# Kernel tuning notes

Measured on AMD Instinct MI355X. Metric: run time of the kernel, lower is better.

Reference implementation:

```python
import jax, jax.numpy as jnp
import numpy as np

N = 50000   # nodes
E = 800000  # edges
F_IN, F_HID, F_OUT = 128, 96, 40


def setup_inputs() -> dict:
    key = jax.random.key(0)
    ks = jax.random.split(key, 9)
    x = jax.random.normal(ks[0], (N, F_IN), dtype=jnp.float32)
    edge_index = jax.random.randint(ks[1], (2, E), 0, N, dtype=jnp.int32)
    def lin(k, fi, fo):
        s = 1.0 / np.sqrt(fi)
        return jax.random.uniform(k, (fi, fo), jnp.float32, -s, s)
    W1 = lin(ks[2], F_IN, F_HID)
    b1 = jnp.zeros((F_HID,), jnp.float32)
    W2 = lin(ks[3], F_HID, F_HID)
    b2 = jnp.zeros((F_HID,), jnp.float32)
    Wout = lin(ks[4], F_HID, F_OUT)
    bout = jnp.zeros((F_OUT,), jnp.float32)
    return {"x": x, "edge_index": edge_index, "W1": W1, "b1": b1,
            "W2": W2, "b2": b2, "Wout": Wout, "bout": bout}


def _gcn_norm(edge_index, n):
    # add self-loops, symmetric degree normalization (PyG GCNConv default)
    loops = jnp.arange(n, dtype=edge_index.dtype)
    src = jnp.concatenate([edge_index[0], loops])
    dst = jnp.concatenate([edge_index[1], loops])
    deg = jax.ops.segment_sum(jnp.ones_like(dst, dtype=jnp.float32), dst,
                              num_segments=n)
    dinv = jnp.where(deg > 0, jax.lax.rsqrt(deg), 0.0)
    norm = dinv[src] * dinv[dst]   # [E+N]
    return src, dst, norm


def _gcn_layer(h, src, dst, norm, W, b, n):
    # linear transform, then normalized scatter-add aggregation, then bias
    h = h @ W                                 # [N, Fout]
    msg = h[src] * norm[:, None]              # gather + scale
    agg = jax.ops.segment_sum(msg, dst, num_segments=n)
    return agg + b


def reference(x, edge_index, W1, b1, W2, b2, Wout, bout):
    n = x.shape[0]
    src, dst, norm = _gcn_norm(edge_index, n)
    h = jax.nn.relu(_gcn_layer(x, src, dst, norm, W1, b1, n))
    h = jax.nn.relu(_gcn_layer(h, src, dst, norm, W2, b2, n))
    return h @ Wout + bout
```

## Files before the change

kernel.cpp:

```cpp
#include <hip/hip_runtime.h>
#include <hip/hip_fp16.h>

#define N_NODES 50000
#define N_EDGES 800000
#define F_INN   128
#define F_HID   96
#define F_OUTT  40


__global__ void count_kernel(const int* __restrict__ dst, int* __restrict__ counts,
                             int* __restrict__ rank, int e) {
    int i = blockIdx.x * blockDim.x + threadIdx.x;
    if (i < e) rank[i] = atomicAdd(&counts[dst[i]], 1);
}

__global__ __launch_bounds__(1024) void scan_local_kernel(
        const int* __restrict__ counts, int* __restrict__ row_start,
        float* __restrict__ dinv, int* __restrict__ blk_sums, int n) {
    __shared__ int wave_sums[16];
    int tid = threadIdx.x, lane = tid & 63, wid = tid >> 6;
    int i = blockIdx.x * 1024 + tid;
    int v = (i < n) ? counts[i] : 0;
    int val = v;
    #pragma unroll
    for (int off = 1; off < 64; off <<= 1) {
        int u = __shfl_up(val, off, 64);
        if (lane >= off) val += u;
    }
    if (lane == 63) wave_sums[wid] = val;
    __syncthreads();
    if (wid == 0) {
        int w = (lane < 16) ? wave_sums[lane] : 0;
        #pragma unroll
        for (int off = 1; off < 16; off <<= 1) {
            int u = __shfl_up(w, off, 64);
            if (lane >= off) w += u;
        }
        if (lane < 16) wave_sums[lane] = w;
    }
    __syncthreads();
    int excl = ((wid == 0) ? 0 : wave_sums[wid - 1]) + (val - v);
    if (i < n) {
        row_start[i] = excl;
        dinv[i] = rsqrtf((float)(v + 1));
    }
    if (tid == 0) blk_sums[blockIdx.x] = wave_sums[15];
}

__global__ void scan_blk_kernel(const int* __restrict__ blk_sums, int* __restrict__ blk_off,
                                int* __restrict__ row_start, int n, int nblk) {
    int lane = threadIdx.x;
    int v = (lane < nblk) ? blk_sums[lane] : 0;
    int val = v;
    #pragma unroll
    for (int off = 1; off < 64; off <<= 1) {
        int u = __shfl_up(val, off, 64);
        if (lane >= off) val += u;
    }
    if (lane < nblk) blk_off[lane] = val - v;
    if (lane == 63) row_start[n] = val;
}

__global__ __launch_bounds__(1024) void scan_apply_kernel(
        int* __restrict__ row_start, const int* __restrict__ blk_off, int n) {
    int i = blockIdx.x * 1024 + threadIdx.x;
    if (i < n) row_start[i] += blk_off[blockIdx.x];
}

__global__ void fill_csr_kernel(const int* __restrict__ src, const int* __restrict__ dst,
                                const int* __restrict__ rank, const int* __restrict__ row_start,
                                int* __restrict__ csr_src, int e) {
    int i = blockIdx.x * blockDim.x + threadIdx.x;
    if (i >= e) return;
    csr_src[row_start[dst[i]] + rank[i]] = src[i];
}


template <int FI>
__global__ __launch_bounds__(384) void gemm96_kernel(
        const float* __restrict__ A, const float* __restrict__ W,
        const float* __restrict__ dinv, __half2* __restrict__ C, int n) {
    __shared__ float Wlds[FI * 96];
    int tid = threadIdx.y * 24 + threadIdx.x;
    for (int i = tid; i < FI * 24; i += 384)
        reinterpret_cast<float4*>(Wlds)[i] = reinterpret_cast<const float4*>(W)[i];
    __syncthreads();

    int j  = threadIdx.x * 4;
    int n0 = blockIdx.x * 64 + threadIdx.y;
    int nn[4];
    #pragma unroll
    for (int t = 0; t < 4; ++t) nn[t] = min(n0 + 16 * t, n - 1);

    float4 acc[4];
    #pragma unroll
    for (int t = 0; t < 4; ++t) acc[t] = make_float4(0.f, 0.f, 0.f, 0.f);

    for (int k = 0; k < FI; k += 4) {
        float4 a[4];
        #pragma unroll
        for (int t = 0; t < 4; ++t)
            a[t] = *reinterpret_cast<const float4*>(A + (size_t)nn[t] * FI + k);
        float4 w0 = *reinterpret_cast<const float4*>(Wlds + (k + 0) * 96 + j);
        float4 w1 = *reinterpret_cast<const float4*>(Wlds + (k + 1) * 96 + j);
        float4 w2 = *reinterpret_cast<const float4*>(Wlds + (k + 2) * 96 + j);
        float4 w3 = *reinterpret_cast<const float4*>(Wlds + (k + 3) * 96 + j);
        #pragma unroll
        for (int t = 0; t < 4; ++t) {
            acc[t].x += a[t].x * w0.x + a[t].y * w1.x + a[t].z * w2.x + a[t].w * w3.x;
            acc[t].y += a[t].x * w0.y + a[t].y * w1.y + a[t].z * w2.y + a[t].w * w3.y;
            acc[t].z += a[t].x * w0.z + a[t].y * w1.z + a[t].z * w2.z + a[t].w * w3.z;
            acc[t].w += a[t].x * w0.w + a[t].y * w1.w + a[t].z * w2.w + a[t].w * w3.w;
        }
    }
    #pragma unroll
    for (int t = 0; t < 4; ++t) {
        int node = n0 + 16 * t;
        if (node < n) {
            float dn = dinv[node];
            __half2 h01 = __floats2half2_rn(acc[t].x * dn, acc[t].y * dn);
            __half2 h23 = __floats2half2_rn(acc[t].z * dn, acc[t].w * dn);
            __half2* Cp = C + (size_t)node * 48 + (j >> 1);
            Cp[0] = h01;
            Cp[1] = h23;
        }
    }
}

__global__ __launch_bounds__(320) void gemm_out_kernel(
        const float* __restrict__ A, const float* __restrict__ W,
        const float* __restrict__ bias, float* __restrict__ C, int n) {
    __shared__ float Wlds[96 * 40];
    int tid = threadIdx.y * 10 + threadIdx.x;
    for (int i = tid; i < 96 * 10; i += 320)
        reinterpret_cast<float4*>(Wlds)[i] = reinterpret_cast<const float4*>(W)[i];
    __syncthreads();

    int j    = threadIdx.x * 4;
    int node = blockIdx.x * 32 + threadIdx.y;
    int nc   = min(node, n - 1);
    float4 acc = make_float4(0.f, 0.f, 0.f, 0.f);
    for (int k = 0; k < 96; k += 4) {
        float4 a = *reinterpret_cast<const float4*>(A + (size_t)nc * 96 + k);
        float4 w0 = *reinterpret_cast<const float4*>(Wlds + (k + 0) * 40 + j);
        float4 w1 = *reinterpret_cast<const float4*>(Wlds + (k + 1) * 40 + j);
        float4 w2 = *reinterpret_cast<const float4*>(Wlds + (k + 2) * 40 + j);
        float4 w3 = *reinterpret_cast<const float4*>(Wlds + (k + 3) * 40 + j);
        acc.x += a.x * w0.x + a.y * w1.x + a.z * w2.x + a.w * w3.x;
        acc.y += a.x * w0.y + a.y * w1.y + a.z * w2.y + a.w * w3.y;
        acc.z += a.x * w0.z + a.y * w1.z + a.z * w2.z + a.w * w3.z;
        acc.w += a.x * w0.w + a.y * w1.w + a.z * w2.w + a.w * w3.w;
    }
    if (node < n) {
        float4 b = *reinterpret_cast<const float4*>(bias + j);
        acc.x += b.x; acc.y += b.y; acc.z += b.z; acc.w += b.w;
        *reinterpret_cast<float4*>(C + (size_t)node * 40 + j) = acc;
    }
}


__global__ __launch_bounds__(256) void agg_kernel(
        const __half2* __restrict__ T, const int* __restrict__ row_start,
        const int* __restrict__ csr_src, const float* __restrict__ dinv,
        const float* __restrict__ bias, float* __restrict__ H, int n) {
    int lane = threadIdx.x & 63;
    int node = __builtin_amdgcn_readfirstlane(blockIdx.x * 4 + (threadIdx.x >> 6));
    if (node >= n) return;
    int fl = min(lane, 47);

    float2 self = __half22float2(T[(size_t)node * 48 + fl]);
    float accx = self.x, accy = self.y;

    int idx = row_start[node];
    int end = row_start[node + 1];
    for (; idx + 4 <= end; idx += 4) {
        int s0 = csr_src[idx + 0];
        int s1 = csr_src[idx + 1];
        int s2 = csr_src[idx + 2];
        int s3 = csr_src[idx + 3];
        __half2 a0 = T[(size_t)s0 * 48 + fl];
        __half2 a1 = T[(size_t)s1 * 48 + fl];
        __half2 a2 = T[(size_t)s2 * 48 + fl];
        __half2 a3 = T[(size_t)s3 * 48 + fl];
        float2 f0 = __half22float2(a0);
        float2 f1 = __half22float2(a1);
        float2 f2 = __half22float2(a2);
        float2 f3 = __half22float2(a3);
        accx += f0.x + f1.x + f2.x + f3.x;
        accy += f0.y + f1.y + f2.y + f3.y;
    }
    for (; idx < end; ++idx) {
        float2 f = __half22float2(T[(size_t)csr_src[idx] * 48 + fl]);
        accx += f.x; accy += f.y;
    }
    if (lane < 48) {
        float dn = dinv[node];
        float2 b = reinterpret_cast<const float2*>(bias)[lane];
        float2 o;
        o.x = fmaxf(dn * accx + b.x, 0.f);
        o.y = fmaxf(dn * accy + b.y, 0.f);
        reinterpret_cast<float2*>(H)[(size_t)node * 48 + lane] = o;
    }
}


extern "C" void kernel_launch(void* const* d_in, const int* in_sizes, int n_in,
                              void* d_out, int out_size, void* d_ws, size_t ws_size,
                              hipStream_t stream) {
    const float* x    = (const float*)d_in[0];
    const int*   ei   = (const int*)d_in[1];
    const float* W1   = (const float*)d_in[2];
    const float* b1   = (const float*)d_in[3];
    const float* W2   = (const float*)d_in[4];
    const float* b2   = (const float*)d_in[5];
    const float* Wout = (const float*)d_in[6];
    const float* bout = (const float*)d_in[7];
    float*       out  = (float*)d_out;

    const int* src = ei;
    const int* dst = ei + N_EDGES;

    char* ws = (char*)d_ws;
    size_t off = 0;
    auto alloc = [&](size_t bytes) {
        size_t o = off;
        off = (off + bytes + 511) & ~(size_t)511;
        return (void*)(ws + o);
    };
    int*     counts    = (int*)    alloc(N_NODES * sizeof(int));
    int*     row_start = (int*)    alloc((N_NODES + 1) * sizeof(int));
    float*   dinv      = (float*)  alloc(N_NODES * sizeof(float));
    int*     blk_sums  = (int*)    alloc(64 * sizeof(int));
    int*     blk_off   = (int*)    alloc(64 * sizeof(int));
    int*     rank      = (int*)    alloc((size_t)N_EDGES * sizeof(int));
    int*     csr_src   = (int*)    alloc((size_t)N_EDGES * sizeof(int));
    __half2* Th        = (__half2*)alloc((size_t)N_NODES * 48 * sizeof(__half2));
    float*   Hf        = (float*)  alloc((size_t)N_NODES * F_HID * sizeof(float));

    const int NSCAN = (N_NODES + 1023) / 1024;

    hipMemsetAsync(counts, 0, N_NODES * sizeof(int), stream);
    count_kernel<<<(N_EDGES + 255) / 256, 256, 0, stream>>>(dst, counts, rank, N_EDGES);
    scan_local_kernel<<<NSCAN, 1024, 0, stream>>>(counts, row_start, dinv, blk_sums, N_NODES);
    scan_blk_kernel<<<1, 64, 0, stream>>>(blk_sums, blk_off, row_start, N_NODES, NSCAN);
    scan_apply_kernel<<<NSCAN, 1024, 0, stream>>>(row_start, blk_off, N_NODES);
    fill_csr_kernel<<<(N_EDGES + 255) / 256, 256, 0, stream>>>(
        src, dst, rank, row_start, csr_src, N_EDGES);

    gemm96_kernel<F_INN><<<(N_NODES + 63) / 64, dim3(24, 16), 0, stream>>>(
        x, W1, dinv, Th, N_NODES);
    agg_kernel<<<(N_NODES + 3) / 4, 256, 0, stream>>>(
        Th, row_start, csr_src, dinv, b1, Hf, N_NODES);

    gemm96_kernel<F_HID><<<(N_NODES + 63) / 64, dim3(24, 16), 0, stream>>>(
        Hf, W2, dinv, Th, N_NODES);
    agg_kernel<<<(N_NODES + 3) / 4, 256, 0, stream>>>(
        Th, row_start, csr_src, dinv, b2, Hf, N_NODES);

    gemm_out_kernel<<<(N_NODES + 31) / 32, dim3(10, 32), 0, stream>>>(
        Hf, Wout, bout, out, N_NODES);
}
```

Baseline: 271.7 us.

## Use MFMA fp16 GEMMs, spread degree-count atomics, unroll aggregation gathers

Replaces the scalar FMA hidden-layer GEMMs with MFMA 16x16x32 fp16 kernels. The weights are pre-transposed to padded fp16 by a new small kernel, and outputs are staged through LDS so the global stores are coalesced. Degree counting now spreads atomics over four sub-counters per node to reduce contention, with per-sub-bucket bases computed in scan_apply. The aggregation inner loop is unrolled from 4 to 8 gathers for more memory-level parallelism. Rounding the GEMM inputs to fp16 adds precision risk.

```diff
diff --git a/kernel.cpp b/kernel.cpp
--- a/kernel.cpp
+++ b/kernel.cpp
@@ -7,20 +7,27 @@
 #define F_HID   96
 #define F_OUTT  40
 
-
-__global__ void count_kernel(const int* __restrict__ dst, int* __restrict__ counts,
+typedef _Float16 half8 __attribute__((ext_vector_type(8)));
+typedef float    floatx4 __attribute__((ext_vector_type(4)));
+
+
+__global__ void count_kernel(const int* __restrict__ dst, int* __restrict__ counts4,
                              int* __restrict__ rank, int e) {
     int i = blockIdx.x * blockDim.x + threadIdx.x;
-    if (i < e) rank[i] = atomicAdd(&counts[dst[i]], 1);
+    if (i < e) rank[i] = atomicAdd(&counts4[dst[i] * 4 + (i & 3)], 1);
 }
 
 __global__ __launch_bounds__(1024) void scan_local_kernel(
-        const int* __restrict__ counts, int* __restrict__ row_start,
+        const int4* __restrict__ counts4, int* __restrict__ row_start,
         float* __restrict__ dinv, int* __restrict__ blk_sums, int n) {
     __shared__ int wave_sums[16];
     int tid = threadIdx.x, lane = tid & 63, wid = tid >> 6;
     int i = blockIdx.x * 1024 + tid;
-    int v = (i < n) ? counts[i] : 0;
+    int v = 0;
+    if (i < n) {
+        int4 c = counts4[i];
+        v = c.x + c.y + c.z + c.w;
+    }
     int val = v;
     #pragma unroll
     for (int off = 1; off < 64; off <<= 1) {
@@ -62,68 +69,95 @@
 }
 
 __global__ __launch_bounds__(1024) void scan_apply_kernel(
-        int* __restrict__ row_start, const int* __restrict__ blk_off, int n) {
+        int* __restrict__ row_start, const int* __restrict__ blk_off,
+        const int4* __restrict__ counts4, int4* __restrict__ base4, int n) {
     int i = blockIdx.x * 1024 + threadIdx.x;
-    if (i < n) row_start[i] += blk_off[blockIdx.x];
+    if (i >= n) return;
+    int4 c = counts4[i];
+    int b = row_start[i] + blk_off[blockIdx.x];
+    row_start[i] = b;
+    base4[i] = make_int4(b, b + c.x, b + c.x + c.y, b + c.x + c.y + c.z);
 }
 
 __global__ void fill_csr_kernel(const int* __restrict__ src, const int* __restrict__ dst,
-                                const int* __restrict__ rank, const int* __restrict__ row_start,
+                                const int* __restrict__ rank, const int* __restrict__ base4,
                                 int* __restrict__ csr_src, int e) {
     int i = blockIdx.x * blockDim.x + threadIdx.x;
     if (i >= e) return;
-    csr_src[row_start[dst[i]] + rank[i]] = src[i];
-}
-
+    csr_src[base4[dst[i] * 4 + (i & 3)] + rank[i]] = src[i];
+}
+
+__global__ void wt_kernel(const float* __restrict__ W1, const float* __restrict__ W2,
+                          __half* __restrict__ BT1, __half* __restrict__ BT2) {
+    int i = blockIdx.x * 256 + threadIdx.x;
+    if (i < 96 * 128) {
+        int j = i / 128, k = i - j * 128;
+        BT1[j * 136 + k] = __float2half(W1[k * 96 + j]);
+    } else if (i < 96 * 128 + 96 * 96) {
+        int t = i - 96 * 128;
+        int j = t / 96, k = t - j * 96;
+        BT2[j * 136 + k] = __float2half(W2[k * 96 + j]);
+    }
+}
 
 template <int FI>
-__global__ __launch_bounds__(384) void gemm96_kernel(
-        const float* __restrict__ A, const float* __restrict__ W,
-        const float* __restrict__ dinv, __half2* __restrict__ C, int n) {
-    __shared__ float Wlds[FI * 96];
-    int tid = threadIdx.y * 24 + threadIdx.x;
-    for (int i = tid; i < FI * 24; i += 384)
-        reinterpret_cast<float4*>(Wlds)[i] = reinterpret_cast<const float4*>(W)[i];
-    __syncthreads();
-
-    int j  = threadIdx.x * 4;
-    int n0 = blockIdx.x * 64 + threadIdx.y;
-    int nn[4];
-    #pragma unroll
-    for (int t = 0; t < 4; ++t) nn[t] = min(n0 + 16 * t, n - 1);
-
-    float4 acc[4];
-    #pragma unroll
-    for (int t = 0; t < 4; ++t) acc[t] = make_float4(0.f, 0.f, 0.f, 0.f);
-
-    for (int k = 0; k < FI; k += 4) {
-        float4 a[4];
-        #pragma unroll
-        for (int t = 0; t < 4; ++t)
-            a[t] = *reinterpret_cast<const float4*>(A + (size_t)nn[t] * FI + k);
-        float4 w0 = *reinterpret_cast<const float4*>(Wlds + (k + 0) * 96 + j);
-        float4 w1 = *reinterpret_cast<const float4*>(Wlds + (k + 1) * 96 + j);
-        float4 w2 = *reinterpret_cast<const float4*>(Wlds + (k + 2) * 96 + j);
-        float4 w3 = *reinterpret_cast<const float4*>(Wlds + (k + 3) * 96 + j);
-        #pragma unroll
-        for (int t = 0; t < 4; ++t) {
-            acc[t].x += a[t].x * w0.x + a[t].y * w1.x + a[t].z * w2.x + a[t].w * w3.x;
-            acc[t].y += a[t].x * w0.y + a[t].y * w1.y + a[t].z * w2.y + a[t].w * w3.y;
-            acc[t].z += a[t].x * w0.z + a[t].y * w1.z + a[t].z * w2.z + a[t].w * w3.z;
-            acc[t].w += a[t].x * w0.w + a[t].y * w1.w + a[t].z * w2.w + a[t].w * w3.w;
+__global__ __launch_bounds__(256) void mfma_gemm_kernel(
+        const float* __restrict__ X, const __half* __restrict__ BTg,
+        const float* __restrict__ dinv, float4* __restrict__ Th4, int n) {
+    __shared__ __half BTl[96 * 136];
+    __shared__ __half OUTl[4 * 16 * 104];
+    int tid = threadIdx.x;
+    {
+        const int4* s = reinterpret_cast<const int4*>(BTg);
+        int4* d = reinterpret_cast<int4*>(BTl);
+        for (int i = tid; i < 96 * 136 / 8; i += 256) d[i] = s[i];
+    }
+    __syncthreads();
+
+    int lane = tid & 63, w = tid >> 6;
+    int lm = lane & 15, q = lane >> 4;
+    int base = blockIdx.x * 64 + w * 16;
+    int node = base + lm;
+    int nclamp = min(node, n - 1);
+    const float* Xrow = X + (size_t)nclamp * FI;
+
+    floatx4 cf[6];
+    #pragma unroll
+    for (int t = 0; t < 6; ++t) cf[t] = (floatx4){0.f, 0.f, 0.f, 0.f};
+
+    constexpr int KS = FI / 32;
+    #pragma unroll
+    for (int ks = 0; ks < KS; ++ks) {
+        const float4* xr = reinterpret_cast<const float4*>(Xrow + 32 * ks + q * 8);
+        float4 f0 = xr[0], f1 = xr[1];
+        union { half8 v; __half2 h[4]; } b;
+        b.h[0] = __floats2half2_rn(f0.x, f0.y);
+        b.h[1] = __floats2half2_rn(f0.z, f0.w);
+        b.h[2] = __floats2half2_rn(f1.x, f1.y);
+        b.h[3] = __floats2half2_rn(f1.z, f1.w);
+        #pragma unroll
+        for (int t = 0; t < 6; ++t) {
+            half8 a = *reinterpret_cast<const half8*>(
+                &BTl[(t * 16 + lm) * 136 + q * 8 + 32 * ks]);
+            cf[t] = __builtin_amdgcn_mfma_f32_16x16x32_f16(a, b.v, cf[t], 0, 0, 0);
         }
     }
-    #pragma unroll
-    for (int t = 0; t < 4; ++t) {
-        int node = n0 + 16 * t;
-        if (node < n) {
-            float dn = dinv[node];
-            __half2 h01 = __floats2half2_rn(acc[t].x * dn, acc[t].y * dn);
-            __half2 h23 = __floats2half2_rn(acc[t].z * dn, acc[t].w * dn);
-            __half2* Cp = C + (size_t)node * 48 + (j >> 1);
-            Cp[0] = h01;
-            Cp[1] = h23;
-        }
+
+    float dn = dinv[nclamp];
+    __half* orow = OUTl + (w * 16 + lm) * 104;
+    #pragma unroll
+    for (int t = 0; t < 6; ++t) {
+        union { int2 i2; __half2 h[2]; } u;
+        u.h[0] = __floats2half2_rn(cf[t][0] * dn, cf[t][1] * dn);
+        u.h[1] = __floats2half2_rn(cf[t][2] * dn, cf[t][3] * dn);
+        *reinterpret_cast<int2*>(&orow[t * 16 + q * 4]) = u.i2;
+    }
+    #pragma unroll
+    for (int R = 0; R < 3; ++R) {
+        int nl = lane >> 2, c = (lane & 3) + 4 * R;
+        float4 v = *reinterpret_cast<const float4*>(&OUTl[(w * 16 + nl) * 104 + c * 8]);
+        int gn = base + nl;
+        if (gn < n) Th4[(size_t)gn * 12 + c] = v;
     }
 }
 
@@ -158,7 +192,6 @@
     }
 }
 
-
 __global__ __launch_bounds__(256) void agg_kernel(
         const __half2* __restrict__ T, const int* __restrict__ row_start,
         const int* __restrict__ csr_src, const float* __restrict__ dinv,
@@ -173,21 +206,15 @@
 
     int idx = row_start[node];
     int end = row_start[node + 1];
-    for (; idx + 4 <= end; idx += 4) {
-        int s0 = csr_src[idx + 0];
-        int s1 = csr_src[idx + 1];
-        int s2 = csr_src[idx + 2];
-        int s3 = csr_src[idx + 3];
-        __half2 a0 = T[(size_t)s0 * 48 + fl];
-        __half2 a1 = T[(size_t)s1 * 48 + fl];
-        __half2 a2 = T[(size_t)s2 * 48 + fl];
-        __half2 a3 = T[(size_t)s3 * 48 + fl];
-        float2 f0 = __half22float2(a0);
-        float2 f1 = __half22float2(a1);
-        float2 f2 = __half22float2(a2);
-        float2 f3 = __half22float2(a3);
-        accx += f0.x + f1.x + f2.x + f3.x;
-        accy += f0.y + f1.y + f2.y + f3.y;
+    for (; idx + 8 <= end; idx += 8) {
+        int s[8];
+        #pragma unroll
+        for (int u = 0; u < 8; ++u) s[u] = csr_src[idx + u];
+        float2 f[8];
+        #pragma unroll
+        for (int u = 0; u < 8; ++u) f[u] = __half22float2(T[(size_t)s[u] * 48 + fl]);
+        #pragma unroll
+        for (int u = 0; u < 8; ++u) { accx += f[u].x; accy += f[u].y; }
     }
     for (; idx < end; ++idx) {
         float2 f = __half22float2(T[(size_t)csr_src[idx] * 48 + fl]);
@@ -227,33 +254,40 @@
         off = (off + bytes + 511) & ~(size_t)511;
         return (void*)(ws + o);
     };
-    int*     counts    = (int*)    alloc(N_NODES * sizeof(int));
+    int*     counts4   = (int*)    alloc((size_t)N_NODES * 4 * sizeof(int));
+    int4*    base4     = (int4*)   alloc((size_t)N_NODES * sizeof(int4));
     int*     row_start = (int*)    alloc((N_NODES + 1) * sizeof(int));
     float*   dinv      = (float*)  alloc(N_NODES * sizeof(float));
     int*     blk_sums  = (int*)    alloc(64 * sizeof(int));
     int*     blk_off   = (int*)    alloc(64 * sizeof(int));
     int*     rank      = (int*)    alloc((size_t)N_EDGES * sizeof(int));
     int*     csr_src   = (int*)    alloc((size_t)N_EDGES * sizeof(int));
+    __half*  BT1       = (__half*) alloc((size_t)96 * 136 * sizeof(__half));
+    __half*  BT2       = (__half*) alloc((size_t)96 * 136 * sizeof(__half));
     __half2* Th        = (__half2*)alloc((size_t)N_NODES * 48 * sizeof(__half2));
     float*   Hf        = (float*)  alloc((size_t)N_NODES * F_HID * sizeof(float));
 
     const int NSCAN = (N_NODES + 1023) / 1024;
 
-    hipMemsetAsync(counts, 0, N_NODES * sizeof(int), stream);
-    count_kernel<<<(N_EDGES + 255) / 256, 256, 0, stream>>>(dst, counts, rank, N_EDGES);
-    scan_local_kernel<<<NSCAN, 1024, 0, stream>>>(counts, row_start, dinv, blk_sums, N_NODES);
+    wt_kernel<<<(96 * 128 + 96 * 96 + 255) / 256, 256, 0, stream>>>(W1, W2, BT1, BT2);
+
+    hipMemsetAsync(counts4, 0, (size_t)N_NODES * 4 * sizeof(int), stream);
+    count_kernel<<<(N_EDGES + 255) / 256, 256, 0, stream>>>(dst, counts4, rank, N_EDGES);
+    scan_local_kernel<<<NSCAN, 1024, 0, stream>>>(
+        (const int4*)counts4, row_start, dinv, blk_sums, N_NODES);
     scan_blk_kernel<<<1, 64, 0, stream>>>(blk_sums, blk_off, row_start, N_NODES, NSCAN);
-    scan_apply_kernel<<<NSCAN, 1024, 0, stream>>>(row_start, blk_off, N_NODES);
+    scan_apply_kernel<<<NSCAN, 1024, 0, stream>>>(
+        row_start, blk_off, (const int4*)counts4, base4, N_NODES);
     fill_csr_kernel<<<(N_EDGES + 255) / 256, 256, 0, stream>>>(
-        src, dst, rank, row_start, csr_src, N_EDGES);
-
-    gemm96_kernel<F_INN><<<(N_NODES + 63) / 64, dim3(24, 16), 0, stream>>>(
-        x, W1, dinv, Th, N_NODES);
+        src, dst, rank, (const int*)base4, csr_src, N_EDGES);
+
+    mfma_gemm_kernel<F_INN><<<(N_NODES + 63) / 64, 256, 0, stream>>>(
+        x, BT1, dinv, (float4*)Th, N_NODES);
     agg_kernel<<<(N_NODES + 3) / 4, 256, 0, stream>>>(
         Th, row_start, csr_src, dinv, b1, Hf, N_NODES);
 
-    gemm96_kernel<F_HID><<<(N_NODES + 63) / 64, dim3(24, 16), 0, stream>>>(
-        Hf, W2, dinv, Th, N_NODES);
+    mfma_gemm_kernel<F_HID><<<(N_NODES + 63) / 64, 256, 0, stream>>>(
+        Hf, BT2, dinv, (float4*)Th, N_NODES);
     agg_kernel<<<(N_NODES + 3) / 4, 256, 0, stream>>>(
         Th, row_start, csr_src, dinv, b2, Hf, N_NODES);
 
```

Measured after the change: 232.6 us. -14.4%, faster.
